# Performance work log

Hardware: AMD Instinct MI355X
Metric: run time of the kernel (lower is better)

Reference implementation:

```python
import jax, jax.numpy as jnp
import numpy as np

HEADS = 16
DIM_HEAD = 64


def setup_inputs() -> dict:
    key = jax.random.key(0)
    k1, k2, k3, k4 = jax.random.split(key, 4)
    b, sq, skv, dim = 2, 2048, 2048, 1024
    inner = HEADS * DIM_HEAD
    return {
        "x_q": jax.random.normal(k1, (b, sq, dim), dtype=jnp.float32),
        "x_kv": jax.random.normal(k2, (b, skv, dim), dtype=jnp.float32),
        "W_qkv": jax.random.normal(k3, (dim, 3 * inner), dtype=jnp.float32) * (dim ** -0.5),
        "W_out": jax.random.normal(k4, (inner, dim), dtype=jnp.float32) * (inner ** -0.5),
        "b_out": jnp.zeros((dim,), dtype=jnp.float32),
    }


def reference(x_q, x_kv, W_qkv, W_out, b_out):
    b, sq, dim = x_q.shape
    skv = x_kv.shape[1]
    inner = HEADS * DIM_HEAD
    scale = DIM_HEAD ** -0.5
    # to_qkv on concat([x_q, x_kv], seq) as in the original (bias-free linear)
    qkv = jnp.concatenate([x_q, x_kv], axis=1) @ W_qkv  # [b, sq+skv, 3*inner]
    q, k, v = jnp.split(qkv, 3, axis=-1)
    q = q[:, :sq].reshape(b, sq, HEADS, DIM_HEAD).transpose(0, 2, 1, 3)   # [b,h,sq,d]
    k = k[:, sq:].reshape(b, skv, HEADS, DIM_HEAD).transpose(0, 2, 1, 3)  # [b,h,skv,d]
    v = v[:, sq:].reshape(b, skv, HEADS, DIM_HEAD).transpose(0, 2, 1, 3)  # [b,h,skv,d]
    dots = jnp.einsum('bhqd,bhkd->bhqk', q, k) * scale
    attn = jax.nn.softmax(dots, axis=-1)  # dropout p=0.0 -> identity
    out = jnp.einsum('bhqk,bhkd->bhqd', attn, v)
    out = out.transpose(0, 2, 1, 3).reshape(b, sq, inner)
    return out @ W_out + b_out
```

## Files before the change

### kernel.cpp

```cpp
#include <hip/hip_runtime.h>


typedef __attribute__((ext_vector_type(8))) short short8;
typedef __attribute__((ext_vector_type(4))) short short4v;
typedef __attribute__((ext_vector_type(4))) float floatx4;

#define QSCALE 0.18033688f

__device__ __forceinline__ ushort f2b(float f) {
  union { float f; unsigned u; } x; x.f = f;
  unsigned r = (x.u + 0x7fffu + ((x.u >> 16) & 1u)) >> 16;
  return (ushort)r;
}

#define GLL(gp, lp)                                                            \
  __builtin_amdgcn_global_load_lds(                                            \
      (const __attribute__((address_space(1))) void*)(gp),                     \
      (__attribute__((address_space(3))) void*)(lp), 16, 0, 0)

__global__ void cvt2(const float* __restrict__ a, const float* __restrict__ bsrc,
                     ushort* __restrict__ oa, ushort* __restrict__ ob, int n) {
  int half = gridDim.x >> 1;
  bool lo = (int)blockIdx.x < half;
  const float* in = lo ? a : bsrc;
  ushort* out = lo ? oa : ob;
  int bid = lo ? blockIdx.x : blockIdx.x - half;
  int stride = half * blockDim.x * 4;
  for (int i = (bid * blockDim.x + threadIdx.x) * 4; i < n; i += stride) {
    float4 v = *(const float4*)(in + i);
    ushort4 o;
    o.x = f2b(v.x); o.y = f2b(v.y); o.z = f2b(v.z); o.w = f2b(v.w);
    *(ushort4*)(out + i) = o;
  }
}

__global__ void transposeW(const float* __restrict__ Wqkv, ushort* __restrict__ WqkvT,
                           const float* __restrict__ Wout, ushort* __restrict__ WoutT) {
  __shared__ float tile[32][33];
  bool first = blockIdx.x < 96;
  const float* in = first ? Wqkv : Wout;
  ushort* out = first ? WqkvT : WoutT;
  int N = first ? 3072 : 1024;
  int bx = first ? blockIdx.x : blockIdx.x - 96;
  int k0 = blockIdx.y * 32, n0 = bx * 32;
  int tx = threadIdx.x, ty = threadIdx.y;
#pragma unroll
  for (int i = 0; i < 32; i += 8)
    tile[ty + i][tx] = in[(size_t)(k0 + ty + i) * N + n0 + tx];
  __syncthreads();
#pragma unroll
  for (int i = 0; i < 32; i += 8)
    out[(size_t)(n0 + ty + i) * 1024 + k0 + tx] = f2b(tile[tx][ty + i]);
}

__global__ __launch_bounds__(256, 3) void gemm_qkv(
    const ushort* __restrict__ Aq, const ushort* __restrict__ Akv,
    const ushort* __restrict__ Bt,
    ushort* __restrict__ Cq, ushort* __restrict__ Ck, ushort* __restrict__ Cv) {
  __shared__ __align__(16) ushort As[2][128 * 32];
  __shared__ __align__(16) ushort Bs[2][128 * 32];
  const int n0 = blockIdx.x * 128, m0 = blockIdx.y * 128;
  const ushort* A = (blockIdx.x >= 8) ? Akv : Aq;
  const int t = threadIdx.x;
  const int w = t >> 6, lane = t & 63, dl = lane & 15, g = lane >> 4;
  const int wm = (w >> 1) * 64, wn = (w & 1) * 64;
  const int K = 1024;

  auto stage = [&](int buf, int k0) {
#pragma unroll
    for (int p = 0; p < 2; p++) {
      int j = t + p * 256;
      int row = j >> 2, slot = j & 3, c = (slot - row) & 3;
      GLL(A + (size_t)(m0 + row) * K + k0 + c * 8, &As[buf][j * 8]);
    }
#pragma unroll
    for (int p = 0; p < 2; p++) {
      int j = t + p * 256;
      int row = j >> 2, slot = j & 3, c = (slot - row) & 3;
      GLL(Bt + (size_t)(n0 + row) * K + k0 + c * 8, &Bs[buf][j * 8]);
    }
  };

  const floatx4 fz = {0.f, 0.f, 0.f, 0.f};
  floatx4 acc[4][4];
#pragma unroll
  for (int i = 0; i < 4; i++)
#pragma unroll
    for (int j = 0; j < 4; j++) acc[i][j] = fz;

  stage(0, 0);
  for (int kt = 0; kt < 32; kt++) {
    int cur = kt & 1;
    __builtin_amdgcn_s_waitcnt(0);
    __syncthreads();
    if (kt + 1 < 32) stage(cur ^ 1, (kt + 1) * 32);
    short8 af[4], bf[4];
#pragma unroll
    for (int mt = 0; mt < 4; mt++) {
      int row = wm + mt * 16 + dl;
      af[mt] = *(const short8*)&As[cur][row * 32 + ((g + row) & 3) * 8];
    }
#pragma unroll
    for (int nt = 0; nt < 4; nt++) {
      int row = wn + nt * 16 + dl;
      bf[nt] = *(const short8*)&Bs[cur][row * 32 + ((g + row) & 3) * 8];
    }
#pragma unroll
    for (int mt = 0; mt < 4; mt++)
#pragma unroll
      for (int nt = 0; nt < 4; nt++)
        acc[mt][nt] = __builtin_amdgcn_mfma_f32_16x16x32_bf16(af[mt], bf[nt], acc[mt][nt], 0, 0, 0);
  }

#pragma unroll
  for (int mt = 0; mt < 4; mt++)
#pragma unroll
    for (int nt = 0; nt < 4; nt++) {
      int gcol = n0 + wn + nt * 16 + dl;
      int row0 = m0 + wm + mt * 16 + g * 4;
      if (gcol < 1024) {
#pragma unroll
        for (int r = 0; r < 4; r++)
          Cq[(size_t)(row0 + r) * 1024 + gcol] = f2b(acc[mt][nt][r] * QSCALE);
      } else if (gcol < 2048) {
#pragma unroll
        for (int r = 0; r < 4; r++)
          Ck[(size_t)(row0 + r) * 1024 + gcol - 1024] = f2b(acc[mt][nt][r]);
      } else {
        short4v pk;
        pk.x = (short)f2b(acc[mt][nt][0]);
        pk.y = (short)f2b(acc[mt][nt][1]);
        pk.z = (short)f2b(acc[mt][nt][2]);
        pk.w = (short)f2b(acc[mt][nt][3]);
        *(short4v*)(Cv + ((size_t)(row0 >> 11) * 1024 + (gcol - 2048)) * 2048 +
                    (row0 & 2047)) = pk;
      }
    }
}

__global__ __launch_bounds__(256, 3) void gemm_out(
    const ushort* __restrict__ A, const ushort* __restrict__ Bt,
    float* __restrict__ C, const float* __restrict__ bias) {
  __shared__ __align__(16) ushort As[2][128 * 64];
  __shared__ __align__(16) ushort Bs[2][64 * 64];
  const int n0 = blockIdx.x * 64, m0 = blockIdx.y * 128;
  const int t = threadIdx.x;
  const int w = t >> 6, lane = t & 63, dl = lane & 15, g = lane >> 4;
  const int wm = (w >> 1) * 64, wn = (w & 1) * 32;
  const int K = 1024;

  auto stage = [&](int buf, int k0) {
#pragma unroll
    for (int p = 0; p < 4; p++) {
      int j = t + p * 256;
      int row = j >> 3, slot = j & 7, c = (slot - row) & 7;
      GLL(A + (size_t)(m0 + row) * K + k0 + c * 8, &As[buf][j * 8]);
    }
#pragma unroll
    for (int p = 0; p < 2; p++) {
      int j = t + p * 256;
      int row = j >> 3, slot = j & 7, c = (slot - row) & 7;
      GLL(Bt + (size_t)(n0 + row) * K + k0 + c * 8, &Bs[buf][j * 8]);
    }
  };

  const floatx4 fz = {0.f, 0.f, 0.f, 0.f};
  floatx4 acc[4][2];
#pragma unroll
  for (int i = 0; i < 4; i++)
#pragma unroll
    for (int j = 0; j < 2; j++) acc[i][j] = fz;

  stage(0, 0);
  for (int kt = 0; kt < 16; kt++) {
    int cur = kt & 1;
    __builtin_amdgcn_s_waitcnt(0);
    __syncthreads();
    if (kt + 1 < 16) stage(cur ^ 1, (kt + 1) * 64);
#pragma unroll
    for (int ks = 0; ks < 2; ks++) {
      short8 af[4], bf[2];
#pragma unroll
      for (int mt = 0; mt < 4; mt++) {
        int row = wm + mt * 16 + dl;
        af[mt] = *(const short8*)&As[cur][row * 64 + ((ks * 4 + g + row) & 7) * 8];
      }
#pragma unroll
      for (int nt = 0; nt < 2; nt++) {
        int row = wn + nt * 16 + dl;
        bf[nt] = *(const short8*)&Bs[cur][row * 64 + ((ks * 4 + g + row) & 7) * 8];
      }
#pragma unroll
      for (int mt = 0; mt < 4; mt++)
#pragma unroll
        for (int nt = 0; nt < 2; nt++)
          acc[mt][nt] = __builtin_amdgcn_mfma_f32_16x16x32_bf16(af[mt], bf[nt], acc[mt][nt], 0, 0, 0);
    }
  }
#pragma unroll
  for (int mt = 0; mt < 4; mt++)
#pragma unroll
    for (int nt = 0; nt < 2; nt++) {
      int gcol = n0 + wn + nt * 16 + dl;
      int row0 = m0 + wm + mt * 16 + g * 4;
      float badd = bias[gcol];
#pragma unroll
      for (int r = 0; r < 4; r++)
        C[(size_t)(row0 + r) * 1024 + gcol] = acc[mt][nt][r] + badd;
    }
}

__global__ __launch_bounds__(256, 4) void attn(
    const ushort* __restrict__ Qb,
    const ushort* __restrict__ Kb,
    const ushort* __restrict__ Vt,
    ushort* __restrict__ Ob) {
  __shared__ __align__(16) ushort Ks[2][64 * 64];
  __shared__ __align__(16) ushort Vs[2][64 * 64];
  __shared__ __align__(16) ushort Pq[64 * 64];

  const int bh = blockIdx.x, b = bh >> 4, h = bh & 15;
  const int q0 = blockIdx.y * 64;
  const int t = threadIdx.x, w = t >> 6, lane = t & 63, dl = lane & 15, g = lane >> 4;
  const int q = w * 16 + dl;

  const ushort* Kg = Kb + (size_t)(b * 2048) * 1024 + h * 64;
  const ushort* Vg = Vt + (size_t)(b * 1024 + h * 64) * 2048;

  const ushort* qrow = Qb + (size_t)(b * 2048 + q0 + q) * 1024 + h * 64;
  short8 bq[2];
  bq[0] = *(const short8*)(qrow + g * 8);
  bq[1] = *(const short8*)(qrow + 32 + g * 8);

  auto stageK = [&](int buf, int kv0) {
#pragma unroll
    for (int p = 0; p < 2; p++) {
      int j = t + p * 256;
      int row = j >> 3, slot = j & 7, c = (slot - row) & 7;
      GLL(Kg + (size_t)(kv0 + row) * 1024 + c * 8, &Ks[buf][j * 8]);
    }
  };
  auto stageV = [&](int buf, int kv0) {
#pragma unroll
    for (int p = 0; p < 2; p++) {
      int j = t + p * 256;
      int row = j >> 3, slot = j & 7, c = (slot - row) & 7;
      GLL(Vg + (size_t)row * 2048 + kv0 + c * 8, &Vs[buf][j * 8]);
    }
  };
  stageK(0, 0);
  stageV(0, 0);

  const floatx4 fz = {0.f, 0.f, 0.f, 0.f};
  floatx4 s[4], o[4];
#pragma unroll
  for (int i = 0; i < 4; i++) o[i] = fz;
  float l_run = 0.f;

  for (int it = 0; it < 32; it++) {
    int cur = it & 1;
    __builtin_amdgcn_s_waitcnt(0);
    __syncthreads();
    if (it + 1 < 32) { stageK(cur ^ 1, (it + 1) * 64); stageV(cur ^ 1, (it + 1) * 64); }

#pragma unroll
    for (int mt = 0; mt < 4; mt++) s[mt] = fz;
#pragma unroll
    for (int ks = 0; ks < 2; ks++) {
      short8 a[4];
#pragma unroll
      for (int mt = 0; mt < 4; mt++) {
        int row = mt * 16 + dl;
        a[mt] = *(const short8*)&Ks[cur][row * 64 + ((ks * 4 + g + row) & 7) * 8];
      }
#pragma unroll
      for (int mt = 0; mt < 4; mt++)
        s[mt] = __builtin_amdgcn_mfma_f32_16x16x32_bf16(a[mt], bq[ks], s[mt], 0, 0, 0);
    }

#pragma unroll
    for (int mt = 0; mt < 4; mt++)
#pragma unroll
      for (int r = 0; r < 4; r++) {
        float pv = exp2f(s[mt][r]);
        s[mt][r] = pv;
        l_run += pv;
      }

#pragma unroll
    for (int mt = 0; mt < 4; mt++) {
      short4v pk;
      pk.x = (short)f2b(s[mt][0]);
      pk.y = (short)f2b(s[mt][1]);
      pk.z = (short)f2b(s[mt][2]);
      pk.w = (short)f2b(s[mt][3]);
      *(short4v*)&Pq[q * 64 + ((mt * 4 + g + q) & 15) * 4] = pk;
    }
    asm volatile("" ::: "memory");

#pragma unroll
    for (int ks2 = 0; ks2 < 2; ks2++) {
      short8 av[4];
#pragma unroll
      for (int mtd = 0; mtd < 4; mtd++) {
        int row = mtd * 16 + dl;
        av[mtd] = *(const short8*)&Vs[cur][row * 64 + ((ks2 * 4 + g + row) & 7) * 8];
      }
      int sq = ks2 * 8 + 2 * g;
      short4v lo = *(const short4v*)&Pq[q * 64 + ((sq + q) & 15) * 4];
      short4v hi = *(const short4v*)&Pq[q * 64 + ((sq + 1 + q) & 15) * 4];
      short8 bp = {lo.x, lo.y, lo.z, lo.w, hi.x, hi.y, hi.z, hi.w};
#pragma unroll
      for (int mtd = 0; mtd < 4; mtd++)
        o[mtd] = __builtin_amdgcn_mfma_f32_16x16x32_bf16(av[mtd], bp, o[mtd], 0, 0, 0);
    }
    asm volatile("" ::: "memory");
  }

  l_run += __shfl_xor(l_run, 16);
  l_run += __shfl_xor(l_run, 32);
  float inv_l = 1.f / l_run;

#pragma unroll
  for (int mtd = 0; mtd < 4; mtd++) {
    short4v pk;
    pk.x = (short)f2b(o[mtd][0] * inv_l);
    pk.y = (short)f2b(o[mtd][1] * inv_l);
    pk.z = (short)f2b(o[mtd][2] * inv_l);
    pk.w = (short)f2b(o[mtd][3] * inv_l);
    *(short4v*)&Pq[q * 64 + ((mtd * 4 + g + q) & 15) * 4] = pk;
  }
  asm volatile("" ::: "memory");
#pragma unroll
  for (int p = 0; p < 2; p++) {
    int j = lane + p * 64;
    int r16 = j >> 3, c = j & 7;
    int qr = w * 16 + r16;
    short4v lo = *(const short4v*)&Pq[qr * 64 + ((2 * c + qr) & 15) * 4];
    short4v hi = *(const short4v*)&Pq[qr * 64 + ((2 * c + 1 + qr) & 15) * 4];
    short8 v = {lo.x, lo.y, lo.z, lo.w, hi.x, hi.y, hi.z, hi.w};
    *(short8*)(Ob + (size_t)(b * 2048 + q0 + qr) * 1024 + h * 64 + c * 8) = v;
  }
}

extern "C" void kernel_launch(void* const* d_in, const int* in_sizes, int n_in,
                              void* d_out, int out_size, void* d_ws, size_t ws_size,
                              hipStream_t stream) {
  const float* x_q  = (const float*)d_in[0];
  const float* x_kv = (const float*)d_in[1];
  const float* Wqkv = (const float*)d_in[2];
  const float* Wout = (const float*)d_in[3];
  const float* bout = (const float*)d_in[4];
  float* out = (float*)d_out;

  char* p = (char*)d_ws;
  ushort* Xq    = (ushort*)p; p += (size_t)4096 * 1024 * 2;
  ushort* Xkv   = (ushort*)p; p += (size_t)4096 * 1024 * 2;
  ushort* WqkvT = (ushort*)p; p += (size_t)3072 * 1024 * 2;
  ushort* WoutT = (ushort*)p; p += (size_t)1024 * 1024 * 2;
  ushort* Qb    = (ushort*)p; p += (size_t)4096 * 1024 * 2;
  ushort* Kb    = (ushort*)p; p += (size_t)4096 * 1024 * 2;
  ushort* Vt    = (ushort*)p; p += (size_t)2 * 1024 * 2048 * 2;
  ushort* Ob    = (ushort*)p; p += (size_t)4096 * 1024 * 2;

  cvt2<<<2048, 256, 0, stream>>>(x_q, x_kv, Xq, Xkv, 4096 * 1024);
  transposeW<<<dim3(128, 32), dim3(32, 8), 0, stream>>>(Wqkv, WqkvT, Wout, WoutT);
  gemm_qkv<<<dim3(24, 32), 256, 0, stream>>>(Xq, Xkv, WqkvT, Qb, Kb, Vt);
  attn<<<dim3(32, 32), 256, 0, stream>>>(Qb, Kb, Vt, Ob);
  gemm_out<<<dim3(16, 32), 256, 0, stream>>>(Ob, WoutT, out, bout);
}
```

Before: 214.5 us.

## Double attention query tile per block and use packed bf16 conversion

The attention kernel now handles 128 queries per block (32 per wave, two 16-row MFMA tiles), so each staged K/V tile in shared memory is reused across twice as many queries. This halves the grid and the total K/V global traffic, but raises register use; launch bounds drop to 2 blocks per SIMD to allow it. A packed two-float-to-bf16 helper built on a byte-permute instruction replaces the scalar conversion in several places. That helper rounds half-up rather than round-to-nearest-even, which changes rounding slightly.

```diff
diff --git a/kernel.cpp b/kernel.cpp
--- a/kernel.cpp
+++ b/kernel.cpp
@@ -11,6 +11,11 @@
   union { float f; unsigned u; } x; x.f = f;
   unsigned r = (x.u + 0x7fffu + ((x.u >> 16) & 1u)) >> 16;
   return (ushort)r;
+}
+
+__device__ __forceinline__ unsigned f2b2(float a, float b) {
+  union { float f; unsigned u; } x, y; x.f = a; y.f = b;
+  return __builtin_amdgcn_perm(y.u + 0x8000u, x.u + 0x8000u, 0x07060302u);
 }
 
 #define GLL(gp, lp)                                                            \
@@ -28,9 +33,10 @@
   int stride = half * blockDim.x * 4;
   for (int i = (bid * blockDim.x + threadIdx.x) * 4; i < n; i += stride) {
     float4 v = *(const float4*)(in + i);
-    ushort4 o;
-    o.x = f2b(v.x); o.y = f2b(v.y); o.z = f2b(v.z); o.w = f2b(v.w);
-    *(ushort4*)(out + i) = o;
+    uint2 o;
+    o.x = f2b2(v.x, v.y);
+    o.y = f2b2(v.z, v.w);
+    *(uint2*)(out + i) = o;
   }
 }
 
@@ -127,13 +133,11 @@
         for (int r = 0; r < 4; r++)
           Ck[(size_t)(row0 + r) * 1024 + gcol - 1024] = f2b(acc[mt][nt][r]);
       } else {
-        short4v pk;
-        pk.x = (short)f2b(acc[mt][nt][0]);
-        pk.y = (short)f2b(acc[mt][nt][1]);
-        pk.z = (short)f2b(acc[mt][nt][2]);
-        pk.w = (short)f2b(acc[mt][nt][3]);
-        *(short4v*)(Cv + ((size_t)(row0 >> 11) * 1024 + (gcol - 2048)) * 2048 +
-                    (row0 & 2047)) = pk;
+        uint2 pk;
+        pk.x = f2b2(acc[mt][nt][0], acc[mt][nt][1]);
+        pk.y = f2b2(acc[mt][nt][2], acc[mt][nt][3]);
+        *(uint2*)(Cv + ((size_t)(row0 >> 11) * 1024 + (gcol - 2048)) * 2048 +
+                  (row0 & 2047)) = pk;
       }
     }
 }
@@ -210,27 +214,30 @@
     }
 }
 
-__global__ __launch_bounds__(256, 4) void attn(
+__global__ __launch_bounds__(256, 2) void attn(
     const ushort* __restrict__ Qb,
     const ushort* __restrict__ Kb,
     const ushort* __restrict__ Vt,
     ushort* __restrict__ Ob) {
   __shared__ __align__(16) ushort Ks[2][64 * 64];
   __shared__ __align__(16) ushort Vs[2][64 * 64];
-  __shared__ __align__(16) ushort Pq[64 * 64];
+  __shared__ __align__(16) ushort Pq[128 * 64];
 
   const int bh = blockIdx.x, b = bh >> 4, h = bh & 15;
-  const int q0 = blockIdx.y * 64;
+  const int q0 = blockIdx.y * 128;
   const int t = threadIdx.x, w = t >> 6, lane = t & 63, dl = lane & 15, g = lane >> 4;
-  const int q = w * 16 + dl;
 
   const ushort* Kg = Kb + (size_t)(b * 2048) * 1024 + h * 64;
   const ushort* Vg = Vt + (size_t)(b * 1024 + h * 64) * 2048;
 
-  const ushort* qrow = Qb + (size_t)(b * 2048 + q0 + q) * 1024 + h * 64;
-  short8 bq[2];
-  bq[0] = *(const short8*)(qrow + g * 8);
-  bq[1] = *(const short8*)(qrow + 32 + g * 8);
+  short8 bq[2][2];
+#pragma unroll
+  for (int nt = 0; nt < 2; nt++) {
+    int qa = q0 + w * 32 + nt * 16 + dl;
+    const ushort* qrow = Qb + (size_t)(b * 2048 + qa) * 1024 + h * 64;
+    bq[nt][0] = *(const short8*)(qrow + g * 8);
+    bq[nt][1] = *(const short8*)(qrow + 32 + g * 8);
+  }
 
   auto stageK = [&](int buf, int kv0) {
 #pragma unroll
@@ -252,10 +259,12 @@
   stageV(0, 0);
 
   const floatx4 fz = {0.f, 0.f, 0.f, 0.f};
-  floatx4 s[4], o[4];
-#pragma unroll
-  for (int i = 0; i < 4; i++) o[i] = fz;
-  float l_run = 0.f;
+  floatx4 o[4][2];
+#pragma unroll
+  for (int i = 0; i < 4; i++)
+#pragma unroll
+    for (int n = 0; n < 2; n++) o[i][n] = fz;
+  float l2[2] = {0.f, 0.f};
 
   for (int it = 0; it < 32; it++) {
     int cur = it & 1;
@@ -263,8 +272,11 @@
     __syncthreads();
     if (it + 1 < 32) { stageK(cur ^ 1, (it + 1) * 64); stageV(cur ^ 1, (it + 1) * 64); }
 
-#pragma unroll
-    for (int mt = 0; mt < 4; mt++) s[mt] = fz;
+    floatx4 s[4][2];
+#pragma unroll
+    for (int mt = 0; mt < 4; mt++)
+#pragma unroll
+      for (int nt = 0; nt < 2; nt++) s[mt][nt] = fz;
 #pragma unroll
     for (int ks = 0; ks < 2; ks++) {
       short8 a[4];
@@ -275,67 +287,86 @@
       }
 #pragma unroll
       for (int mt = 0; mt < 4; mt++)
-        s[mt] = __builtin_amdgcn_mfma_f32_16x16x32_bf16(a[mt], bq[ks], s[mt], 0, 0, 0);
-    }
-
-#pragma unroll
-    for (int mt = 0; mt < 4; mt++)
-#pragma unroll
-      for (int r = 0; r < 4; r++) {
-        float pv = exp2f(s[mt][r]);
-        s[mt][r] = pv;
-        l_run += pv;
-      }
-
-#pragma unroll
-    for (int mt = 0; mt < 4; mt++) {
-      short4v pk;
-      pk.x = (short)f2b(s[mt][0]);
-      pk.y = (short)f2b(s[mt][1]);
-      pk.z = (short)f2b(s[mt][2]);
-      pk.w = (short)f2b(s[mt][3]);
-      *(short4v*)&Pq[q * 64 + ((mt * 4 + g + q) & 15) * 4] = pk;
+#pragma unroll
+        for (int nt = 0; nt < 2; nt++)
+          s[mt][nt] = __builtin_amdgcn_mfma_f32_16x16x32_bf16(a[mt], bq[nt][ks], s[mt][nt], 0, 0, 0);
+    }
+
+#pragma unroll
+    for (int nt = 0; nt < 2; nt++)
+#pragma unroll
+      for (int mt = 0; mt < 4; mt++)
+#pragma unroll
+        for (int r = 0; r < 4; r++) {
+          float pv = exp2f(s[mt][nt][r]);
+          s[mt][nt][r] = pv;
+          l2[nt] += pv;
+        }
+
+#pragma unroll
+    for (int nt = 0; nt < 2; nt++) {
+      int qr = w * 32 + nt * 16 + dl;
+#pragma unroll
+      for (int mt = 0; mt < 4; mt++) {
+        uint2 pk;
+        pk.x = f2b2(s[mt][nt][0], s[mt][nt][1]);
+        pk.y = f2b2(s[mt][nt][2], s[mt][nt][3]);
+        *(uint2*)&Pq[qr * 64 + ((mt * 4 + g + qr) & 15) * 4] = pk;
+      }
     }
     asm volatile("" ::: "memory");
 
 #pragma unroll
     for (int ks2 = 0; ks2 < 2; ks2++) {
-      short8 av[4];
+      short8 av[4], bp[2];
 #pragma unroll
       for (int mtd = 0; mtd < 4; mtd++) {
         int row = mtd * 16 + dl;
         av[mtd] = *(const short8*)&Vs[cur][row * 64 + ((ks2 * 4 + g + row) & 7) * 8];
       }
-      int sq = ks2 * 8 + 2 * g;
-      short4v lo = *(const short4v*)&Pq[q * 64 + ((sq + q) & 15) * 4];
-      short4v hi = *(const short4v*)&Pq[q * 64 + ((sq + 1 + q) & 15) * 4];
-      short8 bp = {lo.x, lo.y, lo.z, lo.w, hi.x, hi.y, hi.z, hi.w};
+#pragma unroll
+      for (int nt = 0; nt < 2; nt++) {
+        int qr = w * 32 + nt * 16 + dl;
+        int sq = ks2 * 8 + 2 * g;
+        short4v lo = *(const short4v*)&Pq[qr * 64 + ((sq + qr) & 15) * 4];
+        short4v hi = *(const short4v*)&Pq[qr * 64 + ((sq + 1 + qr) & 15) * 4];
+        bp[nt] = short8{lo.x, lo.y, lo.z, lo.w, hi.x, hi.y, hi.z, hi.w};
+      }
 #pragma unroll
       for (int mtd = 0; mtd < 4; mtd++)
-        o[mtd] = __builtin_amdgcn_mfma_f32_16x16x32_bf16(av[mtd], bp, o[mtd], 0, 0, 0);
+#pragma unroll
+        for (int nt = 0; nt < 2; nt++)
+          o[mtd][nt] = __builtin_amdgcn_mfma_f32_16x16x32_bf16(av[mtd], bp[nt], o[mtd][nt], 0, 0, 0);
     }
     asm volatile("" ::: "memory");
   }
 
-  l_run += __shfl_xor(l_run, 16);
-  l_run += __shfl_xor(l_run, 32);
-  float inv_l = 1.f / l_run;
-
-#pragma unroll
-  for (int mtd = 0; mtd < 4; mtd++) {
-    short4v pk;
-    pk.x = (short)f2b(o[mtd][0] * inv_l);
-    pk.y = (short)f2b(o[mtd][1] * inv_l);
-    pk.z = (short)f2b(o[mtd][2] * inv_l);
-    pk.w = (short)f2b(o[mtd][3] * inv_l);
-    *(short4v*)&Pq[q * 64 + ((mtd * 4 + g + q) & 15) * 4] = pk;
+  float inv_l[2];
+#pragma unroll
+  for (int nt = 0; nt < 2; nt++) {
+    float l = l2[nt];
+    l += __shfl_xor(l, 16);
+    l += __shfl_xor(l, 32);
+    inv_l[nt] = 1.f / l;
+  }
+
+#pragma unroll
+  for (int nt = 0; nt < 2; nt++) {
+    int qr = w * 32 + nt * 16 + dl;
+#pragma unroll
+    for (int mtd = 0; mtd < 4; mtd++) {
+      uint2 pk;
+      pk.x = f2b2(o[mtd][nt][0] * inv_l[nt], o[mtd][nt][1] * inv_l[nt]);
+      pk.y = f2b2(o[mtd][nt][2] * inv_l[nt], o[mtd][nt][3] * inv_l[nt]);
+      *(uint2*)&Pq[qr * 64 + ((mtd * 4 + g + qr) & 15) * 4] = pk;
+    }
   }
   asm volatile("" ::: "memory");
 #pragma unroll
-  for (int p = 0; p < 2; p++) {
+  for (int p = 0; p < 4; p++) {
     int j = lane + p * 64;
-    int r16 = j >> 3, c = j & 7;
-    int qr = w * 16 + r16;
+    int r32 = j >> 3, c = j & 7;
+    int qr = w * 32 + r32;
     short4v lo = *(const short4v*)&Pq[qr * 64 + ((2 * c + qr) & 15) * 4];
     short4v hi = *(const short4v*)&Pq[qr * 64 + ((2 * c + 1 + qr) & 15) * 4];
     short8 v = {lo.x, lo.y, lo.z, lo.w, hi.x, hi.y, hi.z, hi.w};
@@ -366,6 +397,6 @@
   cvt2<<<2048, 256, 0, stream>>>(x_q, x_kv, Xq, Xkv, 4096 * 1024);
   transposeW<<<dim3(128, 32), dim3(32, 8), 0, stream>>>(Wqkv, WqkvT, Wout, WoutT);
   gemm_qkv<<<dim3(24, 32), 256, 0, stream>>>(Xq, Xkv, WqkvT, Qb, Kb, Vt);
-  attn<<<dim3(32, 32), 256, 0, stream>>>(Qb, Kb, Vt, Ob);
+  attn<<<dim3(32, 16), 256, 0, stream>>>(Qb, Kb, Vt, Ob);
   gemm_out<<<dim3(16, 32), 256, 0, stream>>>(Ob, WoutT, out, bout);
 }
```

Result: no change. 215.4 us (+0.4%).
